# Kernel optimization log

Measured on AMD Instinct MI355X. Metric: run time of the kernel, lower is better.

## Reference

```python
import jax, jax.numpy as jnp
import numpy as np

B_, L_ = 1, 1024
D_MODEL, D_INNER, D_XB = 2048, 4096, 1024
D_STATE = 16
DT_RANK = 128
INTER = 8192
EPS = 1e-5
GC = D_INNER // D_STATE   # 256 state groups (each covers D_STATE channels)
REP = D_INNER // D_XB     # 4: repeat_kv expansion factor for x and B


def setup_inputs() -> dict:
    key = jax.random.key(0)
    ks = jax.random.split(key, 8)
    s = 0.02
    return {
        "hidden_states": jax.random.normal(ks[0], (B_, L_, D_MODEL), jnp.float32),
        "rms1_w": jnp.ones((D_MODEL,), jnp.float32),
        "in_proj_w": jax.random.normal(ks[1], (2 * D_INNER + 2 * D_XB + DT_RANK, D_MODEL), jnp.float32) * s,
        "dt_proj_w": jax.random.normal(ks[2], (D_INNER, DT_RANK), jnp.float32) * s,
        "dt_proj_b": jax.random.normal(ks[3], (D_INNER,), jnp.float32) * 0.5 - 4.0,
        "A_log": jnp.tile(jnp.log(jnp.arange(1, D_STATE + 1, dtype=jnp.float32)), (D_INNER, 1)),
        "D_skip": jnp.ones((D_INNER,), jnp.float32),
        "out_proj_w": jax.random.normal(ks[4], (D_MODEL, D_INNER), jnp.float32) * s,
        "rms2_w": jnp.ones((D_MODEL,), jnp.float32),
        "gate_w": jax.random.normal(ks[5], (INTER, D_MODEL), jnp.float32) * s,
        "up_w": jax.random.normal(ks[6], (INTER, D_MODEL), jnp.float32) * s,
        "down_w": jax.random.normal(ks[7], (D_MODEL, INTER), jnp.float32) * s,
    }


def _rmsnorm(x, w):
    return x * jax.lax.rsqrt(jnp.mean(x * x, axis=-1, keepdims=True) + EPS) * w


def _mamba(x, in_proj_w, dt_proj_w, dt_proj_b, A_log, D_skip, out_proj_w):
    b, l, _ = x.shape
    zxbcdt = x @ in_proj_w.T  # (b,l, 2*d_inner + 2*d_xb + dt_rank)
    z = zxbcdt[..., :D_INNER]
    xv = zxbcdt[..., D_INNER:D_INNER + D_XB]
    Bm = zxbcdt[..., D_INNER + D_XB:D_INNER + 2 * D_XB]
    Cm = zxbcdt[..., D_INNER + 2 * D_XB:2 * D_INNER + 2 * D_XB]
    dt_in = zxbcdt[..., 2 * D_INNER + 2 * D_XB:]
    dt = jax.nn.softplus(dt_in @ dt_proj_w.T + dt_proj_b)  # (b,l,d_inner)
    # repeat_kv-style expansion of x and B from d_xb to d_inner (grouped by d_state)
    xg = jnp.repeat(xv.reshape(b, l, D_XB // D_STATE, D_STATE), REP, axis=2)  # (b,l,GC,n)
    Bg = jnp.repeat(Bm.reshape(b, l, D_XB // D_STATE, D_STATE), REP, axis=2)  # (b,l,GC,n)
    Cg = Cm.reshape(b, l, GC, D_STATE)                                        # (b,l,GC,n)
    x_full = xg.reshape(b, l, D_INNER)
    A = -jnp.exp(A_log)                       # (d_inner, n)
    dA = jnp.exp(dt[..., None] * A)           # (b,l,d_inner,n)
    dtx = (dt * x_full).reshape(b, l, GC, D_INNER // GC)  # channels per group == D_STATE here
    dBx = (dtx[..., :, None] * Bg[..., None, :]).reshape(b, l, D_INNER, D_STATE)

    def step(h, inp):
        dA_i, dBx_i, C_i = inp
        h = dA_i * h + dBx_i                  # (b,d_inner,n)
        # channel d in group d // D_STATE shares C of that group
        y = jnp.einsum('bgn,bgcn->bgc', C_i, h.reshape(b, GC, D_INNER // GC, D_STATE))
        return h, y.reshape(b, D_INNER)

    h0 = jnp.zeros((b, D_INNER, D_STATE), x.dtype)
    _, ys = jax.lax.scan(step, h0, (dA.transpose(1, 0, 2, 3), dBx.transpose(1, 0, 2, 3), Cg.transpose(1, 0, 2, 3)))
    y = ys.transpose(1, 0, 2) + D_skip * x_full
    y = y * jax.nn.silu(z)
    return y @ out_proj_w.T


def reference(hidden_states, rms1_w, in_proj_w, dt_proj_w, dt_proj_b, A_log, D_skip, out_proj_w, rms2_w, gate_w, up_w, down_w):
    res = hidden_states
    h = _rmsnorm(hidden_states, rms1_w)
    h = res + _mamba(h, in_proj_w, dt_proj_w, dt_proj_b, A_log, D_skip, out_proj_w)
    res = h
    hn = _rmsnorm(h, rms2_w)
    mlp = (jax.nn.silu(hn @ gate_w.T) * (hn @ up_w.T)) @ down_w.T
    return res + mlp
```

## Files before the change

### kernel.cpp

```cpp
#include <hip/hip_runtime.h>
#include <cstdint>
#include <cstddef>

#define L_SEQ   1024
#define DMODEL  2048
#define DINNER  4096
#define DXB     1024
#define DSTATE  16
#define DTRANK  128
#define INTER   8192
#define ZROW    10368
#define NCHUNK  64
#define CLEN    16

typedef __attribute__((ext_vector_type(8))) short  short8;
typedef __attribute__((ext_vector_type(4))) float  floatx4;
typedef unsigned short ushort_t;

__device__ __forceinline__ unsigned short f2bf(float f) {
  unsigned u = __float_as_uint(f);
  u += 0x7FFFu + ((u >> 16) & 1u);
  return (unsigned short)(u >> 16);
}
__device__ __forceinline__ float bf2f(unsigned short h) {
  return __uint_as_float(((unsigned)h) << 16);
}

__device__ __forceinline__ void gl_lds16(const void* g, void* l) {
  __builtin_amdgcn_global_load_lds(
      (const __attribute__((address_space(1))) unsigned int*)g,
      (__attribute__((address_space(3))) unsigned int*)l,
      16, 0, 0);
}

__global__ void __launch_bounds__(256) cvt_kernel(
    const float* __restrict__ src, ushort_t* __restrict__ dst, int n8)
{
  int idx = blockIdx.x * 256 + threadIdx.x;
  if (idx < n8) {
    const float4* s = (const float4*)src + (size_t)idx * 2;
    float4 v0 = s[0], v1 = s[1];
    union { ushort_t u[8]; uint4 v; } o;
    o.u[0] = f2bf(v0.x); o.u[1] = f2bf(v0.y); o.u[2] = f2bf(v0.z); o.u[3] = f2bf(v0.w);
    o.u[4] = f2bf(v1.x); o.u[5] = f2bf(v1.y); o.u[6] = f2bf(v1.z); o.u[7] = f2bf(v1.w);
    ((uint4*)dst)[idx] = o.v;
  }
}

template <int MI, int NI, int EPI, bool WF32>
__global__ void __launch_bounds__(256) gemm_bf16(
    const ushort_t* __restrict__ A, int lda,
    const ushort_t* __restrict__ W, int ldw,
    float* __restrict__ C, int ldc, int K,
    const float* __restrict__ aux,
    ushort_t* __restrict__ Cb, int col_lo, int ldcb)
{
  constexpr int BM = MI * 32, BN = NI * 32;
  constexpr int IA = BM / 64, IB = BN / 64;
  constexpr int ASZ = BM * 32, BSZ = BN * 32;
  __shared__ alignas(16) ushort_t As[2 * ASZ];
  __shared__ alignas(16) ushort_t Bs[2 * BSZ];

  const int kz = blockIdx.z;
  A += (size_t)kz * K;
  W += (size_t)kz * K;
  C += (size_t)kz * gridDim.y * BM * ldc;

  const int m0 = blockIdx.y * BM;
  const int n0 = blockIdx.x * BN;
  const int t = threadIdx.x;
  const int lane = t & 63, wave = t >> 6;
  const int wm = wave & 1, wn = wave >> 1;
  const int lrow = lane & 15, quad = lane >> 4;

  const int srow = wave * 16 + (lane >> 2);
  const int skof = (lane & 3) * 8;

  const ushort_t* gA[IA]; ushort_t* lA[IA];
  const ushort_t* gW[IB]; ushort_t* lB[IB];
#pragma unroll
  for (int j = 0; j < IA; ++j) {
    gA[j] = A + (size_t)(m0 + j * 64 + srow) * lda + skof;
    lA[j] = As + j * 2048 + wave * 512;
  }
#pragma unroll
  for (int j = 0; j < IB; ++j) {
    gW[j] = W + (size_t)(n0 + j * 64 + srow) * ldw + skof;
    lB[j] = Bs + j * 2048 + wave * 512;
  }

  floatx4 zero = {0.f, 0.f, 0.f, 0.f};
  floatx4 acc[MI][NI];
#pragma unroll
  for (int a = 0; a < MI; ++a)
#pragma unroll
    for (int b = 0; b < NI; ++b) acc[a][b] = zero;

#pragma unroll
  for (int j = 0; j < IA; ++j) gl_lds16(gA[j], lA[j]);
#pragma unroll
  for (int j = 0; j < IB; ++j) gl_lds16(gW[j], lB[j]);

  int buf = 0;
  for (int k0 = 0; k0 < K; k0 += 32) {
    __syncthreads();
    const int nk = k0 + 32;
    if (nk < K) {
      const int nb = buf ^ 1;
#pragma unroll
      for (int j = 0; j < IA; ++j) gl_lds16(gA[j] + nk, lA[j] + nb * ASZ);
#pragma unroll
      for (int j = 0; j < IB; ++j) gl_lds16(gW[j] + nk, lB[j] + nb * BSZ);
    }

    short8 af[MI], bf_[NI];
#pragma unroll
    for (int mi = 0; mi < MI; ++mi)
      af[mi] = *(const short8*)&As[buf * ASZ + (wm * (MI * 16) + mi * 16 + lrow) * 32 + quad * 8];
#pragma unroll
    for (int ni = 0; ni < NI; ++ni)
      bf_[ni] = *(const short8*)&Bs[buf * BSZ + (wn * (NI * 16) + ni * 16 + lrow) * 32 + quad * 8];
#pragma unroll
    for (int mi = 0; mi < MI; ++mi)
#pragma unroll
      for (int ni = 0; ni < NI; ++ni)
        acc[mi][ni] = __builtin_amdgcn_mfma_f32_16x16x32_bf16(af[mi], bf_[ni], acc[mi][ni], 0, 0, 0);
    buf ^= 1;
  }

#pragma unroll
  for (int mi = 0; mi < MI; ++mi)
#pragma unroll
    for (int ni = 0; ni < NI; ++ni)
#pragma unroll
      for (int reg = 0; reg < 4; ++reg) {
        int row = m0 + wm * (MI * 16) + mi * 16 + quad * 4 + reg;
        int col = n0 + wn * (NI * 16) + ni * 16 + lrow;
        float v = acc[mi][ni][reg];
        if (EPI == 1) {
          v += aux[col];
          v = (v > 20.f) ? v : log1pf(__expf(v));
        }
        if constexpr (WF32)
          C[(size_t)row * ldc + col] = v;
        if (Cb != nullptr && col >= col_lo)
          Cb[(size_t)row * ldcb + (col - col_lo)] = f2bf(v);
      }
}

template <int S>
__global__ void __launch_bounds__(256) reduce_add_kernel(
    const float* __restrict__ part, int stride4,
    const float* __restrict__ aux, float* __restrict__ out, int n4)
{
  int idx = blockIdx.x * 256 + threadIdx.x;
  if (idx < n4) {
    float4 v = ((const float4*)aux)[idx];
#pragma unroll
    for (int s = 0; s < S; ++s) {
      float4 p = ((const float4*)part)[(size_t)s * stride4 + idx];
      v.x += p.x; v.y += p.y; v.z += p.z; v.w += p.w;
    }
    ((float4*)out)[idx] = v;
  }
}

__global__ void __launch_bounds__(256) reduce_rms_kernel(
    const float* __restrict__ part, int stride,
    const float* __restrict__ hidden,
    const float* __restrict__ w,
    float* __restrict__ h2, ushort_t* __restrict__ hn)
{
  const int row = blockIdx.x;
  const int c0 = threadIdx.x * 8;
  float4 v0 = *(const float4*)(hidden + (size_t)row * DMODEL + c0);
  float4 v1 = *(const float4*)(hidden + (size_t)row * DMODEL + c0 + 4);
#pragma unroll
  for (int s = 0; s < 4; ++s) {
    const float* p = part + (size_t)s * stride + (size_t)row * DMODEL + c0;
    float4 p0 = *(const float4*)p;
    float4 p1 = *(const float4*)(p + 4);
    v0.x += p0.x; v0.y += p0.y; v0.z += p0.z; v0.w += p0.w;
    v1.x += p1.x; v1.y += p1.y; v1.z += p1.z; v1.w += p1.w;
  }
  *(float4*)(h2 + (size_t)row * DMODEL + c0)     = v0;
  *(float4*)(h2 + (size_t)row * DMODEL + c0 + 4) = v1;
  float ss = v0.x*v0.x + v0.y*v0.y + v0.z*v0.z + v0.w*v0.w
           + v1.x*v1.x + v1.y*v1.y + v1.z*v1.z + v1.w*v1.w;
#pragma unroll
  for (int off = 32; off > 0; off >>= 1) ss += __shfl_down(ss, off);
  __shared__ float red[5];
  const int lane = threadIdx.x & 63, wv = threadIdx.x >> 6;
  if (lane == 0) red[wv] = ss;
  __syncthreads();
  if (threadIdx.x == 0)
    red[4] = rsqrtf((red[0] + red[1] + red[2] + red[3]) / (float)DMODEL + 1e-5f);
  __syncthreads();
  const float scale = red[4];
  float4 w0 = *(const float4*)(w + c0);
  float4 w1 = *(const float4*)(w + c0 + 4);
  union { ushort_t u[8]; uint4 q; } o;
  o.u[0] = f2bf(v0.x * scale * w0.x); o.u[1] = f2bf(v0.y * scale * w0.y);
  o.u[2] = f2bf(v0.z * scale * w0.z); o.u[3] = f2bf(v0.w * scale * w0.w);
  o.u[4] = f2bf(v1.x * scale * w1.x); o.u[5] = f2bf(v1.y * scale * w1.y);
  o.u[6] = f2bf(v1.z * scale * w1.z); o.u[7] = f2bf(v1.w * scale * w1.w);
  *(uint4*)(hn + (size_t)row * DMODEL + c0) = o.q;
}

__global__ void __launch_bounds__(256) rmsnorm_kernel(
    const float* __restrict__ x, const float* __restrict__ w,
    ushort_t* __restrict__ out)
{
  const int row = blockIdx.x;
  const float* xr = x + (size_t)row * DMODEL;
  float ss = 0.f;
#pragma unroll
  for (int c = threadIdx.x * 4; c < DMODEL; c += 256 * 4) {
    float4 v = *(const float4*)(xr + c);
    ss += v.x * v.x + v.y * v.y + v.z * v.z + v.w * v.w;
  }
#pragma unroll
  for (int off = 32; off > 0; off >>= 1) ss += __shfl_down(ss, off);
  __shared__ float red[5];
  const int lane = threadIdx.x & 63, wv = threadIdx.x >> 6;
  if (lane == 0) red[wv] = ss;
  __syncthreads();
  if (threadIdx.x == 0)
    red[4] = rsqrtf((red[0] + red[1] + red[2] + red[3]) / (float)DMODEL + 1e-5f);
  __syncthreads();
  const float scale = red[4];
  ushort_t* orow = out + (size_t)row * DMODEL;
#pragma unroll
  for (int c = threadIdx.x * 4; c < DMODEL; c += 256 * 4) {
    float4 v  = *(const float4*)(xr + c);
    float4 w4 = *(const float4*)(w + c);
    ushort4 o;
    o.x = f2bf(v.x * scale * w4.x); o.y = f2bf(v.y * scale * w4.y);
    o.z = f2bf(v.z * scale * w4.z); o.w = f2bf(v.w * scale * w4.w);
    *(ushort4*)(orow + c) = o;
  }
}

__global__ void __launch_bounds__(256) scan_phase1(
    const float* __restrict__ zx, const float* __restrict__ dt,
    const float* __restrict__ A_log,
    float* __restrict__ hend, float* __restrict__ sdtb)
{
  const int gt = blockIdx.x * 256 + threadIdx.x;
  const int i  = gt & 4095;
  const int c  = gt >> 12;
  const int l0 = c * CLEN;

  float a[16];
  *(float4*)&a[0]  = *(const float4*)(A_log + i * 16 + 0);
  *(float4*)&a[4]  = *(const float4*)(A_log + i * 16 + 4);
  *(float4*)&a[8]  = *(const float4*)(A_log + i * 16 + 8);
  *(float4*)&a[12] = *(const float4*)(A_log + i * 16 + 12);
#pragma unroll
  for (int n = 0; n < 16; ++n) a[n] = -__expf(a[n]);

  float h[16];
#pragma unroll
  for (int n = 0; n < 16; ++n) h[n] = 0.f;
  float sdt = 0.f;

  const int xci = DINNER + ((i >> 6) << 4) + (i & 15);
  const int bci = DINNER + DXB + ((i >> 6) << 4);
  const float* zr = zx + (size_t)l0 * ZROW;
  const float* dr = dt + (size_t)l0 * DINNER + i;

#pragma unroll 4
  for (int l = 0; l < CLEN; ++l) {
    const float* row = zr + l * ZROW;
    const float d = dr[l * DINNER];
    const float x = row[xci];
    float B[16];
    *(float4*)&B[0]  = *(const float4*)(row + bci);
    *(float4*)&B[4]  = *(const float4*)(row + bci + 4);
    *(float4*)&B[8]  = *(const float4*)(row + bci + 8);
    *(float4*)&B[12] = *(const float4*)(row + bci + 12);
    sdt += d;
    const float dtx = d * x;
#pragma unroll
    for (int n = 0; n < 16; ++n)
      h[n] = __expf(d * a[n]) * h[n] + dtx * B[n];
  }

  float* he = hend + ((size_t)c * 65536 + i * 16);
  *(float4*)(he + 0)  = *(float4*)&h[0];
  *(float4*)(he + 4)  = *(float4*)&h[4];
  *(float4*)(he + 8)  = *(float4*)&h[8];
  *(float4*)(he + 12) = *(float4*)&h[12];
  sdtb[c * 4096 + i] = sdt;
}

__global__ void __launch_bounds__(256) scan_phase2(
    const float* __restrict__ hend, const float* __restrict__ sdtb,
    const float* __restrict__ A_log,
    float* __restrict__ hstart)
{
  const int cs = blockIdx.x * 256 + threadIdx.x;
  const float a = -__expf(A_log[cs]);
  const int i  = cs >> 4;
  float H = 0.f;
#pragma unroll 8
  for (int c = 0; c < NCHUNK; ++c) {
    hstart[c * 65536 + cs] = H;
    H = __expf(a * sdtb[c * 4096 + i]) * H + hend[c * 65536 + cs];
  }
}

__global__ void __launch_bounds__(256) scan_phase3(
    const float* __restrict__ zx, const float* __restrict__ dt,
    const float* __restrict__ A_log, const float* __restrict__ D_skip,
    const float* __restrict__ hstart,
    ushort_t* __restrict__ y)
{
  const int gt = blockIdx.x * 256 + threadIdx.x;
  const int i  = gt & 4095;
  const int c  = gt >> 12;
  const int l0 = c * CLEN;

  float a[16];
  *(float4*)&a[0]  = *(const float4*)(A_log + i * 16 + 0);
  *(float4*)&a[4]  = *(const float4*)(A_log + i * 16 + 4);
  *(float4*)&a[8]  = *(const float4*)(A_log + i * 16 + 8);
  *(float4*)&a[12] = *(const float4*)(A_log + i * 16 + 12);
#pragma unroll
  for (int n = 0; n < 16; ++n) a[n] = -__expf(a[n]);
  const float dsk = D_skip[i];

  float h[16];
  const float* hs = hstart + ((size_t)c * 65536 + i * 16);
  *(float4*)&h[0]  = *(const float4*)(hs + 0);
  *(float4*)&h[4]  = *(const float4*)(hs + 4);
  *(float4*)&h[8]  = *(const float4*)(hs + 8);
  *(float4*)&h[12] = *(const float4*)(hs + 12);

  const int xci = DINNER + ((i >> 6) << 4) + (i & 15);
  const int bci = DINNER + DXB + ((i >> 6) << 4);
  const int cci = DINNER + 2 * DXB + (i & ~15);
  const float* zr = zx + (size_t)l0 * ZROW;
  const float* dr = dt + (size_t)l0 * DINNER + i;
  ushort_t*    py = y + (size_t)l0 * DINNER + i;

#pragma unroll 2
  for (int l = 0; l < CLEN; ++l) {
    const float* row = zr + l * ZROW;
    const float d = dr[l * DINNER];
    const float x = row[xci];
    const float z = row[i];
    float B[16], C[16];
    *(float4*)&B[0]  = *(const float4*)(row + bci);
    *(float4*)&B[4]  = *(const float4*)(row + bci + 4);
    *(float4*)&B[8]  = *(const float4*)(row + bci + 8);
    *(float4*)&B[12] = *(const float4*)(row + bci + 12);
    *(float4*)&C[0]  = *(const float4*)(row + cci);
    *(float4*)&C[4]  = *(const float4*)(row + cci + 4);
    *(float4*)&C[8]  = *(const float4*)(row + cci + 8);
    *(float4*)&C[12] = *(const float4*)(row + cci + 12);
    const float dtx = d * x;
    float p0 = 0.f, p1 = 0.f, p2 = 0.f, p3 = 0.f;
#pragma unroll
    for (int n = 0; n < 4; ++n) {
      h[n]      = __expf(d * a[n])      * h[n]      + dtx * B[n];
      h[n + 4]  = __expf(d * a[n + 4])  * h[n + 4]  + dtx * B[n + 4];
      h[n + 8]  = __expf(d * a[n + 8])  * h[n + 8]  + dtx * B[n + 8];
      h[n + 12] = __expf(d * a[n + 12]) * h[n + 12] + dtx * B[n + 12];
      p0 += C[n] * h[n];
      p1 += C[n + 4] * h[n + 4];
      p2 += C[n + 8] * h[n + 8];
      p3 += C[n + 12] * h[n + 12];
    }
    const float p = (p0 + p1) + (p2 + p3);
    const float sz = z / (1.f + __expf(-z));
    py[l * DINNER] = f2bf((p + dsk * x) * sz);
  }
}

__global__ void __launch_bounds__(256) silu_mul_kernel(
    const ushort_t* __restrict__ g, const ushort_t* __restrict__ u,
    ushort_t* __restrict__ out, int n8)
{
  const int idx = blockIdx.x * 256 + threadIdx.x;
  if (idx < n8) {
    union { uint4 v; ushort_t u[8]; } gv, uv, ov;
    gv.v = ((const uint4*)g)[idx];
    uv.v = ((const uint4*)u)[idx];
#pragma unroll
    for (int j = 0; j < 8; ++j) {
      float gf = bf2f(gv.u[j]), uf = bf2f(uv.u[j]);
      ov.u[j] = f2bf(gf / (1.f + __expf(-gf)) * uf);
    }
    ((uint4*)out)[idx] = ov.v;
  }
}

extern "C" void kernel_launch(void* const* d_in, const int* in_sizes, int n_in,
                              void* d_out, int out_size, void* d_ws, size_t ws_size,
                              hipStream_t stream)
{
  const float* hidden    = (const float*)d_in[0];
  const float* rms1_w    = (const float*)d_in[1];
  const float* in_proj_w = (const float*)d_in[2];
  const float* dt_proj_w = (const float*)d_in[3];
  const float* dt_proj_b = (const float*)d_in[4];
  const float* A_log     = (const float*)d_in[5];
  const float* D_skip    = (const float*)d_in[6];
  const float* out_proj_w= (const float*)d_in[7];
  const float* rms2_w    = (const float*)d_in[8];
  const float* gate_w    = (const float*)d_in[9];
  const float* up_w      = (const float*)d_in[10];
  const float* down_w    = (const float*)d_in[11];
  float* out = (float*)d_out;

  char* ws = (char*)d_ws;
  ushort_t* h_norm_bf = (ushort_t*)(ws + 0);
  float*    h2        = (float*)   (ws + 4194304);
  ushort_t* hn_bf     = (ushort_t*)(ws + 12582912);
  float*    zxbcdt    = (float*)   (ws + 16777216);
  float*    part1     = (float*)   (ws + 16777216);
  ushort_t* gate_bf   = (ushort_t*)(ws + 16777216);
  ushort_t* up_bf     = (ushort_t*)(ws + 33554432);
  ushort_t* hm_bf     = (ushort_t*)(ws + 50331648);
  float*    dtbuf     = (float*)   (ws + 67108864);
  float*    part2     = (float*)   (ws + 67108864);
  float*    hend_s    = (float*)   (ws + 83886080);
  float*    hstart_s  = (float*)   (ws + 100663296);
  float*    sdtb_s    = (float*)   (ws + 117440512);
  ushort_t* ybuf_bf   = (ushort_t*)(ws + 118489088);
  ushort_t* dtA_bf    = (ushort_t*)(ws + 126877696);
  ushort_t* wbuf      = (ushort_t*)(ws + 127139840);

  rmsnorm_kernel<<<L_SEQ, 256, 0, stream>>>(hidden, rms1_w, h_norm_bf);
  cvt_kernel<<<(ZROW * DMODEL / 8 + 255) / 256, 256, 0, stream>>>(in_proj_w, wbuf, ZROW * DMODEL / 8);
  gemm_bf16<4, 4, 0, true><<<dim3(ZROW / 128, L_SEQ / 128, 1), 256, 0, stream>>>(
      h_norm_bf, DMODEL, wbuf, DMODEL, zxbcdt, ZROW, DMODEL, nullptr,
      dtA_bf, 2 * DINNER + 2 * DXB, DTRANK);
  cvt_kernel<<<(DINNER * DTRANK / 8 + 255) / 256, 256, 0, stream>>>(dt_proj_w, wbuf, DINNER * DTRANK / 8);
  gemm_bf16<2, 4, 1, true><<<dim3(DINNER / 128, L_SEQ / 64, 1), 256, 0, stream>>>(
      dtA_bf, DTRANK, wbuf, DTRANK, dtbuf, DINNER, DTRANK, dt_proj_b,
      nullptr, 0, 0);
  scan_phase1<<<1024, 256, 0, stream>>>(zxbcdt, dtbuf, A_log, hend_s, sdtb_s);
  scan_phase2<<<256, 256, 0, stream>>>(hend_s, sdtb_s, A_log, hstart_s);
  scan_phase3<<<1024, 256, 0, stream>>>(zxbcdt, dtbuf, A_log, D_skip, hstart_s, ybuf_bf);
  cvt_kernel<<<(DMODEL * DINNER / 8 + 255) / 256, 256, 0, stream>>>(out_proj_w, wbuf, DMODEL * DINNER / 8);
  gemm_bf16<2, 4, 0, true><<<dim3(DMODEL / 128, L_SEQ / 64, 4), 256, 0, stream>>>(
      ybuf_bf, DINNER, wbuf, DINNER, part1, DMODEL, DINNER / 4, nullptr,
      nullptr, 0, 0);
  reduce_rms_kernel<<<L_SEQ, 256, 0, stream>>>(
      part1, L_SEQ * DMODEL, hidden, rms2_w, h2, hn_bf);
  cvt_kernel<<<(INTER * DMODEL / 8 + 255) / 256, 256, 0, stream>>>(gate_w, wbuf, INTER * DMODEL / 8);
  gemm_bf16<4, 4, 0, false><<<dim3(INTER / 128, L_SEQ / 128, 1), 256, 0, stream>>>(
      hn_bf, DMODEL, wbuf, DMODEL, nullptr, INTER, DMODEL, nullptr,
      gate_bf, 0, INTER);
  cvt_kernel<<<(INTER * DMODEL / 8 + 255) / 256, 256, 0, stream>>>(up_w, wbuf, INTER * DMODEL / 8);
  gemm_bf16<4, 4, 0, false><<<dim3(INTER / 128, L_SEQ / 128, 1), 256, 0, stream>>>(
      hn_bf, DMODEL, wbuf, DMODEL, nullptr, INTER, DMODEL, nullptr,
      up_bf, 0, INTER);
  silu_mul_kernel<<<(L_SEQ * INTER / 8) / 256, 256, 0, stream>>>(
      gate_bf, up_bf, hm_bf, L_SEQ * INTER / 8);
  cvt_kernel<<<(DMODEL * INTER / 8 + 255) / 256, 256, 0, stream>>>(down_w, wbuf, DMODEL * INTER / 8);
  gemm_bf16<2, 4, 0, true><<<dim3(DMODEL / 128, L_SEQ / 64, 4), 256, 0, stream>>>(
      hm_bf, INTER, wbuf, INTER, part2, DMODEL, INTER / 4, nullptr,
      nullptr, 0, 0);
  reduce_add_kernel<4><<<(L_SEQ * DMODEL / 4) / 256, 256, 0, stream>>>(
      part2, L_SEQ * DMODEL / 4, h2, out, L_SEQ * DMODEL / 4);
}
```

Measured before the change: 681.2 us.

## Use 4-stage ring-buffered GEMM with LDS swizzle, XCD remap, fused gate/up GEMM

Replaces the double-buffered GEMM with a single 128x128 kernel that keeps a 4-slot LDS ring with three tiles in flight, using explicit vmcnt waits. It also XOR-swizzles LDS chunks to avoid bank conflicts and remaps workgroup IDs so neighbouring tiles land on the same XCD. The gate and up projections are merged into one GEMM over concatenated weights, with an adjusted silu-mul. The intent is to hide global-load latency and cut launch and cache overhead. The cost is more LDS per block and fewer blocks for the small GEMMs (dt_proj, split-K), which may reduce occupancy.

```diff
diff --git a/kernel.cpp b/kernel.cpp
--- a/kernel.cpp
+++ b/kernel.cpp
@@ -47,102 +47,116 @@
   }
 }
 
-template <int MI, int NI, int EPI, bool WF32>
-__global__ void __launch_bounds__(256) gemm_bf16(
+template <int EPI, bool WF32>
+__global__ void __launch_bounds__(256, 2) gemm_ring(
     const ushort_t* __restrict__ A, int lda,
     const ushort_t* __restrict__ W, int ldw,
     float* __restrict__ C, int ldc, int K,
     const float* __restrict__ aux,
     ushort_t* __restrict__ Cb, int col_lo, int ldcb)
 {
-  constexpr int BM = MI * 32, BN = NI * 32;
-  constexpr int IA = BM / 64, IB = BN / 64;
-  constexpr int ASZ = BM * 32, BSZ = BN * 32;
-  __shared__ alignas(16) ushort_t As[2 * ASZ];
-  __shared__ alignas(16) ushort_t Bs[2 * BSZ];
-
-  const int kz = blockIdx.z;
+  constexpr int ASZ = 128 * 32;
+  __shared__ alignas(16) ushort_t As[4 * ASZ];
+  __shared__ alignas(16) ushort_t Bs[4 * ASZ];
+
+  const int gx = gridDim.x, gy = gridDim.y;
+  const int nwg = gx * gy * (int)gridDim.z;
+  const int id  = ((int)blockIdx.z * gy + (int)blockIdx.y) * gx + (int)blockIdx.x;
+  const int q = nwg >> 3, r = nwg & 7, xc = id & 7, dd = id >> 3;
+  const int wg = (xc < r ? xc * (q + 1) : r * (q + 1) + (xc - r) * q) + dd;
+  const int bx  = wg % gx;
+  const int byz = wg / gx;
+  const int by  = byz % gy;
+  const int kz  = byz / gy;
+
   A += (size_t)kz * K;
   W += (size_t)kz * K;
-  C += (size_t)kz * gridDim.y * BM * ldc;
-
-  const int m0 = blockIdx.y * BM;
-  const int n0 = blockIdx.x * BN;
+  float* Cz = nullptr;
+  if constexpr (WF32) Cz = C + (size_t)kz * gy * 128 * ldc;
+
+  const int m0 = by * 128, n0 = bx * 128;
   const int t = threadIdx.x;
   const int lane = t & 63, wave = t >> 6;
   const int wm = wave & 1, wn = wave >> 1;
   const int lrow = lane & 15, quad = lane >> 4;
+  const int chunk = (quad ^ (lrow & 3)) << 3;
 
   const int srow = wave * 16 + (lane >> 2);
-  const int skof = (lane & 3) * 8;
-
-  const ushort_t* gA[IA]; ushort_t* lA[IA];
-  const ushort_t* gW[IB]; ushort_t* lB[IB];
-#pragma unroll
-  for (int j = 0; j < IA; ++j) {
-    gA[j] = A + (size_t)(m0 + j * 64 + srow) * lda + skof;
-    lA[j] = As + j * 2048 + wave * 512;
-  }
-#pragma unroll
-  for (int j = 0; j < IB; ++j) {
-    gW[j] = W + (size_t)(n0 + j * 64 + srow) * ldw + skof;
-    lB[j] = Bs + j * 2048 + wave * 512;
-  }
+  const int skof = (((lane & 3) ^ ((lane >> 2) & 3)) << 3);
+
+  const ushort_t* gA0 = A + (size_t)(m0 +  0 + srow) * lda + skof;
+  const ushort_t* gA1 = A + (size_t)(m0 + 64 + srow) * lda + skof;
+  const ushort_t* gW0 = W + (size_t)(n0 +  0 + srow) * ldw + skof;
+  const ushort_t* gW1 = W + (size_t)(n0 + 64 + srow) * ldw + skof;
+  ushort_t* lA0 = As + wave * 512;
+  ushort_t* lA1 = As + 2048 + wave * 512;
+  ushort_t* lB0 = Bs + wave * 512;
+  ushort_t* lB1 = Bs + 2048 + wave * 512;
 
   floatx4 zero = {0.f, 0.f, 0.f, 0.f};
-  floatx4 acc[MI][NI];
-#pragma unroll
-  for (int a = 0; a < MI; ++a)
-#pragma unroll
-    for (int b = 0; b < NI; ++b) acc[a][b] = zero;
-
-#pragma unroll
-  for (int j = 0; j < IA; ++j) gl_lds16(gA[j], lA[j]);
-#pragma unroll
-  for (int j = 0; j < IB; ++j) gl_lds16(gW[j], lB[j]);
-
-  int buf = 0;
-  for (int k0 = 0; k0 < K; k0 += 32) {
-    __syncthreads();
-    const int nk = k0 + 32;
-    if (nk < K) {
-      const int nb = buf ^ 1;
-#pragma unroll
-      for (int j = 0; j < IA; ++j) gl_lds16(gA[j] + nk, lA[j] + nb * ASZ);
-#pragma unroll
-      for (int j = 0; j < IB; ++j) gl_lds16(gW[j] + nk, lB[j] + nb * BSZ);
+  floatx4 acc[4][4];
+#pragma unroll
+  for (int a = 0; a < 4; ++a)
+#pragma unroll
+    for (int b = 0; b < 4; ++b) acc[a][b] = zero;
+
+  const int T = K >> 5;
+
+#pragma unroll
+  for (int p = 0; p < 3; ++p) {
+    const int ko = p * 32, s = p * ASZ;
+    gl_lds16(gA0 + ko, lA0 + s);
+    gl_lds16(gA1 + ko, lA1 + s);
+    gl_lds16(gW0 + ko, lB0 + s);
+    gl_lds16(gW1 + ko, lB1 + s);
+  }
+
+  for (int tt = 0; tt < T; ++tt) {
+    if (tt + 2 < T)      asm volatile("s_waitcnt vmcnt(8)" ::: "memory");
+    else if (tt + 1 < T) asm volatile("s_waitcnt vmcnt(4)" ::: "memory");
+    else                 asm volatile("s_waitcnt vmcnt(0)" ::: "memory");
+    __builtin_amdgcn_s_barrier();
+    __builtin_amdgcn_sched_barrier(0);
+
+    if (tt + 3 < T) {
+      const int ko = (tt + 3) * 32;
+      const int s  = ((tt + 3) & 3) * ASZ;
+      gl_lds16(gA0 + ko, lA0 + s);
+      gl_lds16(gA1 + ko, lA1 + s);
+      gl_lds16(gW0 + ko, lB0 + s);
+      gl_lds16(gW1 + ko, lB1 + s);
     }
 
-    short8 af[MI], bf_[NI];
-#pragma unroll
-    for (int mi = 0; mi < MI; ++mi)
-      af[mi] = *(const short8*)&As[buf * ASZ + (wm * (MI * 16) + mi * 16 + lrow) * 32 + quad * 8];
-#pragma unroll
-    for (int ni = 0; ni < NI; ++ni)
-      bf_[ni] = *(const short8*)&Bs[buf * BSZ + (wn * (NI * 16) + ni * 16 + lrow) * 32 + quad * 8];
-#pragma unroll
-    for (int mi = 0; mi < MI; ++mi)
-#pragma unroll
-      for (int ni = 0; ni < NI; ++ni)
+    const int cs = (tt & 3) * ASZ;
+    short8 af[4], bf_[4];
+#pragma unroll
+    for (int mi = 0; mi < 4; ++mi)
+      af[mi] = *(const short8*)&As[cs + (wm * 64 + mi * 16 + lrow) * 32 + chunk];
+#pragma unroll
+    for (int ni = 0; ni < 4; ++ni)
+      bf_[ni] = *(const short8*)&Bs[cs + (wn * 64 + ni * 16 + lrow) * 32 + chunk];
+#pragma unroll
+    for (int mi = 0; mi < 4; ++mi)
+#pragma unroll
+      for (int ni = 0; ni < 4; ++ni)
         acc[mi][ni] = __builtin_amdgcn_mfma_f32_16x16x32_bf16(af[mi], bf_[ni], acc[mi][ni], 0, 0, 0);
-    buf ^= 1;
-  }
-
-#pragma unroll
-  for (int mi = 0; mi < MI; ++mi)
-#pragma unroll
-    for (int ni = 0; ni < NI; ++ni)
+  }
+
+#pragma unroll
+  for (int mi = 0; mi < 4; ++mi)
+#pragma unroll
+    for (int ni = 0; ni < 4; ++ni)
 #pragma unroll
       for (int reg = 0; reg < 4; ++reg) {
-        int row = m0 + wm * (MI * 16) + mi * 16 + quad * 4 + reg;
-        int col = n0 + wn * (NI * 16) + ni * 16 + lrow;
+        int row = m0 + wm * 64 + mi * 16 + quad * 4 + reg;
+        int col = n0 + wn * 64 + ni * 16 + lrow;
         float v = acc[mi][ni][reg];
         if (EPI == 1) {
           v += aux[col];
           v = (v > 20.f) ? v : log1pf(__expf(v));
         }
         if constexpr (WF32)
-          C[(size_t)row * ldc + col] = v;
+          Cz[(size_t)row * ldc + col] = v;
         if (Cb != nullptr && col >= col_lo)
           Cb[(size_t)row * ldcb + (col - col_lo)] = f2bf(v);
       }
@@ -378,21 +392,23 @@
   }
 }
 
-__global__ void __launch_bounds__(256) silu_mul_kernel(
-    const ushort_t* __restrict__ g, const ushort_t* __restrict__ u,
-    ushort_t* __restrict__ out, int n8)
+__global__ void __launch_bounds__(256) silu_mul2_kernel(
+    const ushort_t* __restrict__ gu, ushort_t* __restrict__ out, int n8)
 {
   const int idx = blockIdx.x * 256 + threadIdx.x;
   if (idx < n8) {
+    const int row = idx >> 10;
+    const int j   = (idx & 1023) << 3;
+    const ushort_t* gp = gu + (size_t)row * (2 * INTER) + j;
     union { uint4 v; ushort_t u[8]; } gv, uv, ov;
-    gv.v = ((const uint4*)g)[idx];
-    uv.v = ((const uint4*)u)[idx];
-#pragma unroll
-    for (int j = 0; j < 8; ++j) {
-      float gf = bf2f(gv.u[j]), uf = bf2f(uv.u[j]);
-      ov.u[j] = f2bf(gf / (1.f + __expf(-gf)) * uf);
+    gv.v = *(const uint4*)gp;
+    uv.v = *(const uint4*)(gp + INTER);
+#pragma unroll
+    for (int jj = 0; jj < 8; ++jj) {
+      float gf = bf2f(gv.u[jj]), uf = bf2f(uv.u[jj]);
+      ov.u[jj] = f2bf(gf / (1.f + __expf(-gf)) * uf);
     }
-    ((uint4*)out)[idx] = ov.v;
+    *(uint4*)(out + (size_t)row * INTER + j) = ov.v;
   }
 }
 
@@ -420,10 +436,10 @@
   ushort_t* hn_bf     = (ushort_t*)(ws + 12582912);
   float*    zxbcdt    = (float*)   (ws + 16777216);
   float*    part1     = (float*)   (ws + 16777216);
-  ushort_t* gate_bf   = (ushort_t*)(ws + 16777216);
-  ushort_t* up_bf     = (ushort_t*)(ws + 33554432);
+  ushort_t* gu_bf     = (ushort_t*)(ws + 16777216);
   ushort_t* hm_bf     = (ushort_t*)(ws + 50331648);
   float*    dtbuf     = (float*)   (ws + 67108864);
+  ushort_t* guw_bf    = (ushort_t*)(ws + 67108864);
   float*    part2     = (float*)   (ws + 67108864);
   float*    hend_s    = (float*)   (ws + 83886080);
   float*    hstart_s  = (float*)   (ws + 100663296);
@@ -434,34 +450,31 @@
 
   rmsnorm_kernel<<<L_SEQ, 256, 0, stream>>>(hidden, rms1_w, h_norm_bf);
   cvt_kernel<<<(ZROW * DMODEL / 8 + 255) / 256, 256, 0, stream>>>(in_proj_w, wbuf, ZROW * DMODEL / 8);
-  gemm_bf16<4, 4, 0, true><<<dim3(ZROW / 128, L_SEQ / 128, 1), 256, 0, stream>>>(
+  gemm_ring<0, true><<<dim3(ZROW / 128, L_SEQ / 128, 1), 256, 0, stream>>>(
       h_norm_bf, DMODEL, wbuf, DMODEL, zxbcdt, ZROW, DMODEL, nullptr,
       dtA_bf, 2 * DINNER + 2 * DXB, DTRANK);
   cvt_kernel<<<(DINNER * DTRANK / 8 + 255) / 256, 256, 0, stream>>>(dt_proj_w, wbuf, DINNER * DTRANK / 8);
-  gemm_bf16<2, 4, 1, true><<<dim3(DINNER / 128, L_SEQ / 64, 1), 256, 0, stream>>>(
+  gemm_ring<1, true><<<dim3(DINNER / 128, L_SEQ / 128, 1), 256, 0, stream>>>(
       dtA_bf, DTRANK, wbuf, DTRANK, dtbuf, DINNER, DTRANK, dt_proj_b,
       nullptr, 0, 0);
   scan_phase1<<<1024, 256, 0, stream>>>(zxbcdt, dtbuf, A_log, hend_s, sdtb_s);
   scan_phase2<<<256, 256, 0, stream>>>(hend_s, sdtb_s, A_log, hstart_s);
   scan_phase3<<<1024, 256, 0, stream>>>(zxbcdt, dtbuf, A_log, D_skip, hstart_s, ybuf_bf);
   cvt_kernel<<<(DMODEL * DINNER / 8 + 255) / 256, 256, 0, stream>>>(out_proj_w, wbuf, DMODEL * DINNER / 8);
-  gemm_bf16<2, 4, 0, true><<<dim3(DMODEL / 128, L_SEQ / 64, 4), 256, 0, stream>>>(
+  gemm_ring<0, true><<<dim3(DMODEL / 128, L_SEQ / 128, 4), 256, 0, stream>>>(
       ybuf_bf, DINNER, wbuf, DINNER, part1, DMODEL, DINNER / 4, nullptr,
       nullptr, 0, 0);
   reduce_rms_kernel<<<L_SEQ, 256, 0, stream>>>(
       part1, L_SEQ * DMODEL, hidden, rms2_w, h2, hn_bf);
-  cvt_kernel<<<(INTER * DMODEL / 8 + 255) / 256, 256, 0, stream>>>(gate_w, wbuf, INTER * DMODEL / 8);
-  gemm_bf16<4, 4, 0, false><<<dim3(INTER / 128, L_SEQ / 128, 1), 256, 0, stream>>>(
-      hn_bf, DMODEL, wbuf, DMODEL, nullptr, INTER, DMODEL, nullptr,
-      gate_bf, 0, INTER);
-  cvt_kernel<<<(INTER * DMODEL / 8 + 255) / 256, 256, 0, stream>>>(up_w, wbuf, INTER * DMODEL / 8);
-  gemm_bf16<4, 4, 0, false><<<dim3(INTER / 128, L_SEQ / 128, 1), 256, 0, stream>>>(
-      hn_bf, DMODEL, wbuf, DMODEL, nullptr, INTER, DMODEL, nullptr,
-      up_bf, 0, INTER);
-  silu_mul_kernel<<<(L_SEQ * INTER / 8) / 256, 256, 0, stream>>>(
-      gate_bf, up_bf, hm_bf, L_SEQ * INTER / 8);
+  cvt_kernel<<<(INTER * DMODEL / 8 + 255) / 256, 256, 0, stream>>>(gate_w, guw_bf, INTER * DMODEL / 8);
+  cvt_kernel<<<(INTER * DMODEL / 8 + 255) / 256, 256, 0, stream>>>(up_w, guw_bf + (size_t)INTER * DMODEL, INTER * DMODEL / 8);
+  gemm_ring<0, false><<<dim3(2 * INTER / 128, L_SEQ / 128, 1), 256, 0, stream>>>(
+      hn_bf, DMODEL, guw_bf, DMODEL, nullptr, 0, DMODEL, nullptr,
+      gu_bf, 0, 2 * INTER);
+  silu_mul2_kernel<<<(L_SEQ * INTER / 8) / 256, 256, 0, stream>>>(
+      gu_bf, hm_bf, L_SEQ * INTER / 8);
   cvt_kernel<<<(DMODEL * INTER / 8 + 255) / 256, 256, 0, stream>>>(down_w, wbuf, DMODEL * INTER / 8);
-  gemm_bf16<2, 4, 0, true><<<dim3(DMODEL / 128, L_SEQ / 64, 4), 256, 0, stream>>>(
+  gemm_ring<0, true><<<dim3(DMODEL / 128, L_SEQ / 128, 4), 256, 0, stream>>>(
       hm_bf, INTER, wbuf, INTER, part2, DMODEL, INTER / 4, nullptr,
       nullptr, 0, 0);
   reduce_add_kernel<4><<<(L_SEQ * DMODEL / 4) / 256, 256, 0, stream>>>(
```

After: 707.8 us. 1.04x slower.
